# Optimization experiments

Measured on AMD Instinct MI355X. Metric: run time of the kernel, lower is better.

## Reference

```python
import jax, jax.numpy as jnp
import numpy as np

N_GRAPHS = 64
NODES_PER_GRAPH = 1024
N_NODES = N_GRAPHS * NODES_PER_GRAPH
AVG_DEGREE = 32
N_EDGES = N_NODES * AVG_DEGREE
D_FEAT = 256
ALPHA = 0.5
RATIO = 0.5
K = max(int(RATIO * NODES_PER_GRAPH), 1)  # 512 kept nodes per graph


def setup_inputs() -> dict:
    key = jax.random.key(0)
    ks = jax.random.split(key, 6)
    x = jax.random.normal(ks[0], (N_NODES, D_FEAT), dtype=jnp.float32)
    # intra-graph random edges (src, dst local in [0, n), offset by graph id)
    epg = N_EDGES // N_GRAPHS
    src_loc = jax.random.randint(ks[1], (N_EDGES,), 0, NODES_PER_GRAPH, dtype=jnp.int32)
    dst_loc = jax.random.randint(ks[2], (N_EDGES,), 0, NODES_PER_GRAPH, dtype=jnp.int32)
    off = (jnp.arange(N_EDGES, dtype=jnp.int32) // epg) * NODES_PER_GRAPH
    edge_index = jnp.stack([src_loc + off, dst_loc + off])  # [2, E] int32
    batch = jnp.repeat(jnp.arange(N_GRAPHS, dtype=jnp.int32), NODES_PER_GRAPH)
    scale = 1.0 / np.sqrt(D_FEAT)
    w1 = jax.random.normal(ks[3], (D_FEAT, 1), dtype=jnp.float32) * scale
    b1 = jnp.zeros((1,), dtype=jnp.float32)
    wg = jax.random.normal(ks[4], (D_FEAT, 1), dtype=jnp.float32) * scale
    bg = jnp.zeros((1,), dtype=jnp.float32)
    return {"x": x, "edge_index": edge_index, "batch": batch,
            "w1": w1, "b1": b1, "wg": wg, "bg": bg}


def reference(x, edge_index, batch, w1, b1, wg, bg):
    N = x.shape[0]
    row, col = edge_index[0], edge_index[1]
    # remove_self_loops only affects the GCN scoring path
    ew = (row != col).astype(x.dtype)  # zero-weight self loops == removed
    # GCNConv (add_self_loops=False): D^-1/2 A D^-1/2 (X Wg) + bg
    deg = jnp.zeros((N,), x.dtype).at[col].add(ew)
    dis = jnp.where(deg > 0, jax.lax.rsqrt(jnp.maximum(deg, 1.0)), 0.0)
    norm = dis[row] * dis[col] * ew  # [E]
    xw = x @ wg  # [N, 1]
    gcn = jnp.zeros((N, 1), x.dtype).at[col].add(norm[:, None] * xw[row]) + bg
    score = (ALPHA * (x @ w1 + b1) + (1.0 - ALPHA) * gcn).squeeze(-1)  # [N]
    # segmented top-k: equal-sized graphs -> reshape to [B, n]
    sc = score.reshape(N_GRAPHS, NODES_PER_GRAPH)
    _, idx = jax.lax.top_k(sc, K)  # [B, K], descending (matches torch.topk order)
    perm = (idx + (jnp.arange(N_GRAPHS, dtype=idx.dtype) * NODES_PER_GRAPH)[:, None]).reshape(-1)
    x_new = x[perm] * jnp.tanh(score[perm])[:, None]  # [B*K, D]
    batch_new = batch[perm]
    # filter_adj: keep edges with both endpoints selected, relabel by position in perm
    node_map = jnp.full((N,), -1, jnp.int32).at[perm].set(jnp.arange(perm.shape[0], dtype=jnp.int32))
    er, ec = node_map[row], node_map[col]
    valid = (er >= 0) & (ec >= 0)
    new_edge_index = jnp.where(valid[None, :], jnp.stack([er, ec]), -1)  # -1 marks dropped edges
    return x_new, new_edge_index, batch_new
```

## Files before the change

kernel.cpp:

```cpp
#include <hip/hip_runtime.h>

#define NPG 1024
#define NG 64
#define KKEEP 512
#define DF 256
#define NTOT (NG * NPG)
#define NROWS (NG * KKEEP)
#define EPG 32768
#define NBD 4
#define EPBD (EPG / NBD)
#define NB 8
#define EPB (EPG / NB)
#define HI_ROWS 256
#define LO_ROWS (NROWS - HI_ROWS)
#define FXS 1099511627776.0
#define DOTS_BLOCKS (NTOT / 16)

typedef float vf4 __attribute__((ext_vector_type(4)));
typedef int   vi4 __attribute__((ext_vector_type(4)));
typedef unsigned int vu4 __attribute__((ext_vector_type(4)));

__device__ __forceinline__ unsigned long long cex(unsigned long long a, int t, int k, int j) {
    unsigned long long b = __shfl_xor(a, j, 64);
    bool lower = ((t & j) == 0);
    bool desc  = ((t & k) == 0);
    unsigned long long mn = a < b ? a : b;
    unsigned long long mx = a < b ? b : a;
    return (desc == lower) ? mx : mn;
}

__global__ __launch_bounds__(256) void k_front(const float* __restrict__ x,
                                               const float* __restrict__ w1,
                                               const float* __restrict__ wg,
                                               const int* __restrict__ rows,
                                               const int* __restrict__ cols,
                                               float* __restrict__ sc0,
                                               float* __restrict__ xwg,
                                               int* __restrict__ degp,
                                               unsigned int* __restrict__ ep) {
    __shared__ int deg_l[NPG];
    const int b = blockIdx.x;
    const int t = threadIdx.x;
    if (b < DOTS_BLOCKS) {
        const int lane = t & 63;
        const int grp  = lane & 15;
        const int node = b * 16 + (t >> 6) * 4 + (lane >> 4);
        double s1 = 0.0, s2 = 0.0;
#pragma unroll
        for (int i = 0; i < 4; ++i) {
            const int off = grp * 4 + i * 64;
            const float4 xv = *reinterpret_cast<const float4*>(x + (size_t)node * DF + off);
            const float4 av = *reinterpret_cast<const float4*>(w1 + off);
            const float4 bv = *reinterpret_cast<const float4*>(wg + off);
            s1 += (double)xv.x * av.x + (double)xv.y * av.y + (double)xv.z * av.z + (double)xv.w * av.w;
            s2 += (double)xv.x * bv.x + (double)xv.y * bv.y + (double)xv.z * bv.z + (double)xv.w * bv.w;
        }
#pragma unroll
        for (int m = 1; m <= 8; m <<= 1) {
            s1 += __shfl_xor(s1, m);
            s2 += __shfl_xor(s2, m);
        }
        if (grp == 0) { sc0[node] = (float)s1; xwg[node] = (float)s2; }
    } else {
        const int bb = b - DOTS_BLOCKS;
        const int g = bb >> 2, sub = bb & 3;
        deg_l[t] = 0; deg_l[t + 256] = 0; deg_l[t + 512] = 0; deg_l[t + 768] = 0;
        __syncthreads();
        const size_t e0 = (size_t)g * EPG + sub * EPBD;
        const int4* r4 = reinterpret_cast<const int4*>(rows + e0);
        const int4* c4 = reinterpret_cast<const int4*>(cols + e0);
        vu4* ep4 = reinterpret_cast<vu4*>(ep + e0);
#pragma unroll 2
        for (int i = t; i < EPBD / 4; i += 256) {
            int4 r = r4[i], c = c4[i];
            vu4 p;
            p.x = (((unsigned)r.x & (NPG - 1)) << 10) | ((unsigned)c.x & (NPG - 1));
            p.y = (((unsigned)r.y & (NPG - 1)) << 10) | ((unsigned)c.y & (NPG - 1));
            p.z = (((unsigned)r.z & (NPG - 1)) << 10) | ((unsigned)c.z & (NPG - 1));
            p.w = (((unsigned)r.w & (NPG - 1)) << 10) | ((unsigned)c.w & (NPG - 1));
            ep4[i] = p;
            if (r.x != c.x) atomicAdd(&deg_l[p.x & (NPG - 1)], 1);
            if (r.y != c.y) atomicAdd(&deg_l[p.y & (NPG - 1)], 1);
            if (r.z != c.z) atomicAdd(&deg_l[p.z & (NPG - 1)], 1);
            if (r.w != c.w) atomicAdd(&deg_l[p.w & (NPG - 1)], 1);
        }
        __syncthreads();
        int* dst = degp + (size_t)bb * NPG;
        dst[t] = deg_l[t]; dst[t + 256] = deg_l[t + 256];
        dst[t + 512] = deg_l[t + 512]; dst[t + 768] = deg_l[t + 768];
    }
}

__global__ __launch_bounds__(1024) void k_gcn(const unsigned int* __restrict__ ep,
                                              const int* __restrict__ degp,
                                              const float* __restrict__ xwg,
                                              unsigned long long* __restrict__ gcnp) {
    __shared__ float dis_l[NPG];
    __shared__ float dxw_l[NPG];
    __shared__ unsigned long long gcn_l[NPG];
    const int t = threadIdx.x;
    const int g = blockIdx.x >> 3, sub = blockIdx.x & 7;
    {
        int d = degp[(size_t)(g * NBD + 0) * NPG + t] + degp[(size_t)(g * NBD + 1) * NPG + t]
              + degp[(size_t)(g * NBD + 2) * NPG + t] + degp[(size_t)(g * NBD + 3) * NPG + t];
        float dis = (d > 0) ? (1.0f / sqrtf((float)d)) : 0.0f;
        dis_l[t] = dis;
        dxw_l[t] = dis * xwg[g * NPG + t];
    }
    gcn_l[t] = 0;
    __syncthreads();
    const vu4* ep4 = reinterpret_cast<const vu4*>(ep + (size_t)g * EPG + sub * EPB);
    for (int i = t; i < EPB / 4; i += 1024) {
        vu4 p = ep4[i];
        int rl, cl; float term;
        rl = (p.x >> 10) & (NPG - 1); cl = p.x & (NPG - 1);
        if (rl != cl) { term = dxw_l[rl] * dis_l[cl];
            atomicAdd(&gcn_l[cl], (unsigned long long)(long long)llrint((double)term * FXS)); }
        rl = (p.y >> 10) & (NPG - 1); cl = p.y & (NPG - 1);
        if (rl != cl) { term = dxw_l[rl] * dis_l[cl];
            atomicAdd(&gcn_l[cl], (unsigned long long)(long long)llrint((double)term * FXS)); }
        rl = (p.z >> 10) & (NPG - 1); cl = p.z & (NPG - 1);
        if (rl != cl) { term = dxw_l[rl] * dis_l[cl];
            atomicAdd(&gcn_l[cl], (unsigned long long)(long long)llrint((double)term * FXS)); }
        rl = (p.w >> 10) & (NPG - 1); cl = p.w & (NPG - 1);
        if (rl != cl) { term = dxw_l[rl] * dis_l[cl];
            atomicAdd(&gcn_l[cl], (unsigned long long)(long long)llrint((double)term * FXS)); }
    }
    __syncthreads();
    gcnp[(size_t)blockIdx.x * NPG + t] = gcn_l[t];
}

__global__ __launch_bounds__(1024) void k_sort(const float* __restrict__ sc0,
                                               const unsigned long long* __restrict__ gcnp,
                                               const float* __restrict__ b1,
                                               const float* __restrict__ bg,
                                               int* __restrict__ node_map,
                                               int2* __restrict__ rowinfo) {
    __shared__ unsigned long long keys[NPG];
    __shared__ float score_l[NPG];
    const int g = blockIdx.x, t = threadIdx.x;
    const int nbase = g * NPG;
    unsigned long long key;
    {
        long long q = 0;
#pragma unroll
        for (int p = 0; p < NB; ++p) q += (long long)gcnp[(size_t)(g * NB + p) * NPG + t];
        float s2 = (float)((double)q * (1.0 / FXS)) + bg[0];
        float s1 = sc0[nbase + t] + b1[0];
        float s = 0.5f * s1 + 0.5f * s2;
        score_l[t] = s;
        unsigned u = __float_as_uint(s);
        u = (u & 0x80000000u) ? ~u : (u | 0x80000000u);
        key = ((unsigned long long)u << 32) | (unsigned long long)(0xFFFFFFFFu - (unsigned)t);
    }
#pragma unroll
    for (int k = 2; k <= 64; k <<= 1)
        for (int j = k >> 1; j > 0; j >>= 1)
            key = cex(key, t, k, j);
    keys[t] = key;
    __syncthreads();
    for (int k = 128; k <= NPG; k <<= 1) {
        for (int j = k >> 1; j >= 64; j >>= 1) {
            int ixj = t ^ j;
            if (ixj > t) {
                unsigned long long a = keys[t], b = keys[ixj];
                bool desc = ((t & k) == 0);
                if (desc ? (a < b) : (a > b)) { keys[t] = b; keys[ixj] = a; }
            }
            __syncthreads();
        }
        key = keys[t];
#pragma unroll
        for (int j = 32; j > 0; j >>= 1)
            key = cex(key, t, k, j);
        if (k < NPG) { keys[t] = key; __syncthreads(); }
    }
    int idx = (int)(0xFFFFFFFFu - (unsigned)(key & 0xFFFFFFFFull)) & (NPG - 1);
    if (t < KKEEP) {
        int row = g * KKEEP + t;
        node_map[nbase + idx] = row;
        rowinfo[row] = make_int2(nbase + idx, __float_as_int(tanhf(score_l[idx])));
    } else {
        node_map[nbase + idx] = -1;
    }
}

__device__ __forceinline__ void edge_body_packed(const unsigned int* __restrict__ ep,
                                                 const int* __restrict__ node_map,
                                                 float* __restrict__ oute, int E, int i) {
    const int* nm = node_map + (i >> 13) * NPG;
    vu4 p = __builtin_nontemporal_load(reinterpret_cast<const vu4*>(ep) + i);
    int ex = nm[(p.x >> 10) & (NPG - 1)], fx = nm[p.x & (NPG - 1)];
    int ey = nm[(p.y >> 10) & (NPG - 1)], fy = nm[p.y & (NPG - 1)];
    int ez = nm[(p.z >> 10) & (NPG - 1)], fz = nm[p.z & (NPG - 1)];
    int ew = nm[(p.w >> 10) & (NPG - 1)], fw = nm[p.w & (NPG - 1)];
    vf4 orow, ocol;
    orow.x = (ex >= 0 && fx >= 0) ? (float)ex : -1.0f;  ocol.x = (ex >= 0 && fx >= 0) ? (float)fx : -1.0f;
    orow.y = (ey >= 0 && fy >= 0) ? (float)ey : -1.0f;  ocol.y = (ey >= 0 && fy >= 0) ? (float)fy : -1.0f;
    orow.z = (ez >= 0 && fz >= 0) ? (float)ez : -1.0f;  ocol.z = (ez >= 0 && fz >= 0) ? (float)fz : -1.0f;
    orow.w = (ew >= 0 && fw >= 0) ? (float)ew : -1.0f;  ocol.w = (ew >= 0 && fw >= 0) ? (float)fw : -1.0f;
    __builtin_nontemporal_store(orow, reinterpret_cast<vf4*>(oute) + i);
    __builtin_nontemporal_store(ocol, reinterpret_cast<vf4*>(oute + (size_t)E) + i);
}

__device__ __forceinline__ void edge_body_raw(const int* __restrict__ rows,
                                              const int* __restrict__ cols,
                                              const int* __restrict__ node_map,
                                              float* __restrict__ oute, int E, int i) {
    vi4 r = __builtin_nontemporal_load(reinterpret_cast<const vi4*>(rows) + i);
    vi4 c = __builtin_nontemporal_load(reinterpret_cast<const vi4*>(cols) + i);
    int ex = node_map[r.x & (NTOT - 1)], fx = node_map[c.x & (NTOT - 1)];
    int ey = node_map[r.y & (NTOT - 1)], fy = node_map[c.y & (NTOT - 1)];
    int ez = node_map[r.z & (NTOT - 1)], fz = node_map[c.z & (NTOT - 1)];
    int ew = node_map[r.w & (NTOT - 1)], fw = node_map[c.w & (NTOT - 1)];
    vf4 orow, ocol;
    orow.x = (ex >= 0 && fx >= 0) ? (float)ex : -1.0f;  ocol.x = (ex >= 0 && fx >= 0) ? (float)fx : -1.0f;
    orow.y = (ey >= 0 && fy >= 0) ? (float)ey : -1.0f;  ocol.y = (ey >= 0 && fy >= 0) ? (float)fy : -1.0f;
    orow.z = (ez >= 0 && fz >= 0) ? (float)ez : -1.0f;  ocol.z = (ez >= 0 && fz >= 0) ? (float)fz : -1.0f;
    orow.w = (ew >= 0 && fw >= 0) ? (float)ew : -1.0f;  ocol.w = (ew >= 0 && fw >= 0) ? (float)fw : -1.0f;
    __builtin_nontemporal_store(orow, reinterpret_cast<vf4*>(oute) + i);
    __builtin_nontemporal_store(ocol, reinterpret_cast<vf4*>(oute + (size_t)E) + i);
}

__device__ __forceinline__ void gather_row(const float* __restrict__ x, int2 ri, int row,
                                           float* __restrict__ outx, float* __restrict__ outb,
                                           int lane) {
    float tg = __int_as_float(ri.y);
    const float4 v = *reinterpret_cast<const float4*>(x + (size_t)(ri.x & (NTOT - 1)) * DF + lane * 4);
    vf4 o;
    o.x = v.x * tg; o.y = v.y * tg; o.z = v.z * tg; o.w = v.w * tg;
    __builtin_nontemporal_store(o, reinterpret_cast<vf4*>(outx + (size_t)row * DF) + lane);
    if (lane == 0) __builtin_nontemporal_store((float)(row >> 9), outb + row);
}

__global__ __launch_bounds__(256) void k_out(const float* __restrict__ x,
                                             const unsigned int* __restrict__ ep,
                                             const int* __restrict__ rows,
                                             const int* __restrict__ cols,
                                             const int* __restrict__ node_map,
                                             const int2* __restrict__ rowinfo,
                                             float* __restrict__ outx,
                                             float* __restrict__ oute,
                                             float* __restrict__ outb, int E) {
    const int b = blockIdx.x, t = threadIdx.x;
    if (b < NROWS / 4) {
        int row = b * 4 + (t >> 6);
        gather_row(x, rowinfo[row], row, outx, outb, t & 63);
    } else {
        int i = (b - NROWS / 4) * 256 + t;
        if (i < E / 4) {
            if (ep) edge_body_packed(ep, node_map, oute, E, i);
            else    edge_body_raw(rows, cols, node_map, oute, E, i);
        }
    }
}

__global__ __launch_bounds__(256) void k_edges(const unsigned int* __restrict__ ep,
                                               const int* __restrict__ node_map,
                                               float* __restrict__ oute, int E) {
    int i = blockIdx.x * blockDim.x + threadIdx.x;
    if (i < E / 4) edge_body_packed(ep, node_map, oute, E, i);
}

__global__ __launch_bounds__(256) void k_gather(const float* __restrict__ x,
                                                const int2* __restrict__ rowinfo,
                                                float* __restrict__ outx,
                                                float* __restrict__ outb) {
    int row = blockIdx.x * 4 + (threadIdx.x >> 6);
    gather_row(x, rowinfo[row], row, outx, outb, threadIdx.x & 63);
}

__global__ __launch_bounds__(1024) void k_gather_hi(const float* __restrict__ x,
                                                    const int2* __restrict__ rowinfo,
                                                    float* __restrict__ outx,
                                                    float* __restrict__ outb) {
    __shared__ int2 info[HI_ROWS];
    int tid = threadIdx.x;
    if (tid < HI_ROWS) info[tid] = rowinfo[LO_ROWS + tid];
    __syncthreads();
    for (int it = tid; it < HI_ROWS * 64; it += 1024) {
        int rl = it >> 6, lane = it & 63;
        gather_row(x, info[rl], LO_ROWS + rl, outx, outb, lane);
    }
}

extern "C" void kernel_launch(void* const* d_in, const int* in_sizes, int n_in,
                              void* d_out, int out_size, void* d_ws, size_t ws_size,
                              hipStream_t stream) {
    const float* x = (const float*)d_in[0];
    const int* ei = (const int*)d_in[1];
    const float* w1 = (const float*)d_in[3];
    const float* b1 = (const float*)d_in[4];
    const float* wg = (const float*)d_in[5];
    const float* bg = (const float*)d_in[6];

    const int N = in_sizes[0] / DF;
    const int E = in_sizes[1] / 2;
    const int* rows = ei;
    const int* cols = ei + E;

    float* outx = (float*)d_out;
    float* oute = outx + (size_t)NROWS * DF;
    float* outb = oute + (size_t)2 * E;

    char* sb = (char*)d_out;
    float*              sc0  = (float*)(sb + 0);
    float*              xwg  = (float*)(sb + (1 << 18));
    int*                degp = (int*)(sb + (2 << 18));
    unsigned long long* gcnp = (unsigned long long*)(sb + (6 << 18));

    const size_t EPBYTES = (size_t)E * 4;
    int tier;
    int*  node_map;
    int2* rowinfo;
    unsigned int* ep;
    unsigned int* ep_out;
    if (ws_size >= (size_t)NTOT * 4 + (size_t)NROWS * 8 + EPBYTES) {
        tier = 1;
        node_map = (int*)d_ws;
        rowinfo  = (int2*)((char*)d_ws + (size_t)NTOT * 4);
        ep       = (unsigned int*)((char*)d_ws + (size_t)NTOT * 4 + (size_t)NROWS * 8);
        ep_out   = ep;
    } else if (ws_size >= (size_t)NTOT * 4 + (size_t)NROWS * 8) {
        tier = 1;
        node_map = (int*)d_ws;
        rowinfo  = (int2*)((char*)d_ws + (size_t)NTOT * 4);
        ep       = (unsigned int*)(sb + (22 << 18));
        ep_out   = nullptr;
    } else if (ws_size >= (size_t)NROWS * 8) {
        tier = 2;
        node_map = (int*)(sb + (54 << 18));
        rowinfo  = (int2*)d_ws;
        ep       = (unsigned int*)(sb + (22 << 18));
        ep_out   = ep;
    } else {
        tier = 3;
        node_map = (int*)(sb + (54 << 18));
        rowinfo  = (int2*)(sb + (size_t)NROWS * DF * 4 - (size_t)NROWS * 8);
        ep       = (unsigned int*)(sb + (22 << 18));
        ep_out   = ep;
    }

    hipLaunchKernelGGL(k_front, dim3(DOTS_BLOCKS + NG * NBD), dim3(256), 0, stream,
                       x, w1, wg, rows, cols, sc0, xwg, degp, ep);
    hipLaunchKernelGGL(k_gcn, dim3(NG * NB), dim3(1024), 0, stream, ep, degp, xwg, gcnp);
    hipLaunchKernelGGL(k_sort, dim3(NG), dim3(1024), 0, stream, sc0, gcnp, b1, bg, node_map, rowinfo);
    if (tier == 1) {
        hipLaunchKernelGGL(k_out, dim3(NROWS / 4 + E / 4 / 256), dim3(256), 0, stream,
                           x, ep_out, rows, cols, node_map, rowinfo, outx, oute, outb, E);
    } else if (tier == 2) {
        hipLaunchKernelGGL(k_edges, dim3(E / 4 / 256), dim3(256), 0, stream, ep_out, node_map, oute, E);
        hipLaunchKernelGGL(k_gather, dim3(NROWS / 4), dim3(256), 0, stream, x, rowinfo, outx, outb);
    } else {
        hipLaunchKernelGGL(k_edges, dim3(E / 4 / 256), dim3(256), 0, stream, ep_out, node_map, oute, E);
        hipLaunchKernelGGL(k_gather, dim3(LO_ROWS / 4), dim3(256), 0, stream, x, rowinfo, outx, outb);
        hipLaunchKernelGGL(k_gather_hi, dim3(1), dim3(1024), 0, stream, x, rowinfo, outx, outb);
    }
}
```

Measured before the change: 52.67 us.

## Fuse GCN aggregation and per-graph sort into one kernel per graph

Merges the GCN scatter kernel (8 blocks per graph) and the top-k sort kernel into a single kernel with one 1024-thread block per graph. The gcn partial sums stay in shared memory, and that buffer is reused for the sort keys. This removes the gcnp round trip through global memory and one kernel launch. The cost is less parallelism for the edge aggregation: 64 blocks instead of 512, each walking 32K edges. Edge index loads in k_front are also switched to nontemporal loads.

```diff
diff --git a/kernel.cpp b/kernel.cpp
--- a/kernel.cpp
+++ b/kernel.cpp
@@ -9,8 +9,6 @@
 #define EPG 32768
 #define NBD 4
 #define EPBD (EPG / NBD)
-#define NB 8
-#define EPB (EPG / NB)
 #define HI_ROWS 256
 #define LO_ROWS (NROWS - HI_ROWS)
 #define FXS 1099511627776.0
@@ -67,12 +65,13 @@
         deg_l[t] = 0; deg_l[t + 256] = 0; deg_l[t + 512] = 0; deg_l[t + 768] = 0;
         __syncthreads();
         const size_t e0 = (size_t)g * EPG + sub * EPBD;
-        const int4* r4 = reinterpret_cast<const int4*>(rows + e0);
-        const int4* c4 = reinterpret_cast<const int4*>(cols + e0);
+        const vi4* r4 = reinterpret_cast<const vi4*>(rows + e0);
+        const vi4* c4 = reinterpret_cast<const vi4*>(cols + e0);
         vu4* ep4 = reinterpret_cast<vu4*>(ep + e0);
 #pragma unroll 2
         for (int i = t; i < EPBD / 4; i += 256) {
-            int4 r = r4[i], c = c4[i];
+            vi4 r = __builtin_nontemporal_load(r4 + i);
+            vi4 c = __builtin_nontemporal_load(c4 + i);
             vu4 p;
             p.x = (((unsigned)r.x & (NPG - 1)) << 10) | ((unsigned)c.x & (NPG - 1));
             p.y = (((unsigned)r.y & (NPG - 1)) << 10) | ((unsigned)c.y & (NPG - 1));
@@ -91,26 +90,31 @@
     }
 }
 
-__global__ __launch_bounds__(1024) void k_gcn(const unsigned int* __restrict__ ep,
-                                              const int* __restrict__ degp,
-                                              const float* __restrict__ xwg,
-                                              unsigned long long* __restrict__ gcnp) {
+__global__ __launch_bounds__(1024) void k_gs(const unsigned int* __restrict__ ep,
+                                             const int* __restrict__ degp,
+                                             const float* __restrict__ xwg,
+                                             const float* __restrict__ sc0,
+                                             const float* __restrict__ b1,
+                                             const float* __restrict__ bg,
+                                             int* __restrict__ node_map,
+                                             int2* __restrict__ rowinfo) {
     __shared__ float dis_l[NPG];
     __shared__ float dxw_l[NPG];
     __shared__ unsigned long long gcn_l[NPG];
-    const int t = threadIdx.x;
-    const int g = blockIdx.x >> 3, sub = blockIdx.x & 7;
+    __shared__ float score_l[NPG];
+    const int g = blockIdx.x, t = threadIdx.x;
+    const int nbase = g * NPG;
     {
         int d = degp[(size_t)(g * NBD + 0) * NPG + t] + degp[(size_t)(g * NBD + 1) * NPG + t]
               + degp[(size_t)(g * NBD + 2) * NPG + t] + degp[(size_t)(g * NBD + 3) * NPG + t];
         float dis = (d > 0) ? (1.0f / sqrtf((float)d)) : 0.0f;
         dis_l[t] = dis;
-        dxw_l[t] = dis * xwg[g * NPG + t];
+        dxw_l[t] = dis * xwg[nbase + t];
     }
     gcn_l[t] = 0;
     __syncthreads();
-    const vu4* ep4 = reinterpret_cast<const vu4*>(ep + (size_t)g * EPG + sub * EPB);
-    for (int i = t; i < EPB / 4; i += 1024) {
+    const vu4* ep4 = reinterpret_cast<const vu4*>(ep + (size_t)g * EPG);
+    for (int i = t; i < EPG / 4; i += 1024) {
         vu4 p = ep4[i];
         int rl, cl; float term;
         rl = (p.x >> 10) & (NPG - 1); cl = p.x & (NPG - 1);
@@ -127,25 +131,9 @@
             atomicAdd(&gcn_l[cl], (unsigned long long)(long long)llrint((double)term * FXS)); }
     }
     __syncthreads();
-    gcnp[(size_t)blockIdx.x * NPG + t] = gcn_l[t];
-}
-
-__global__ __launch_bounds__(1024) void k_sort(const float* __restrict__ sc0,
-                                               const unsigned long long* __restrict__ gcnp,
-                                               const float* __restrict__ b1,
-                                               const float* __restrict__ bg,
-                                               int* __restrict__ node_map,
-                                               int2* __restrict__ rowinfo) {
-    __shared__ unsigned long long keys[NPG];
-    __shared__ float score_l[NPG];
-    const int g = blockIdx.x, t = threadIdx.x;
-    const int nbase = g * NPG;
     unsigned long long key;
     {
-        long long q = 0;
-#pragma unroll
-        for (int p = 0; p < NB; ++p) q += (long long)gcnp[(size_t)(g * NB + p) * NPG + t];
-        float s2 = (float)((double)q * (1.0 / FXS)) + bg[0];
+        float s2 = (float)((double)(long long)gcn_l[t] * (1.0 / FXS)) + bg[0];
         float s1 = sc0[nbase + t] + b1[0];
         float s = 0.5f * s1 + 0.5f * s2;
         score_l[t] = s;
@@ -157,23 +145,23 @@
     for (int k = 2; k <= 64; k <<= 1)
         for (int j = k >> 1; j > 0; j >>= 1)
             key = cex(key, t, k, j);
-    keys[t] = key;
+    gcn_l[t] = key;
     __syncthreads();
     for (int k = 128; k <= NPG; k <<= 1) {
         for (int j = k >> 1; j >= 64; j >>= 1) {
             int ixj = t ^ j;
             if (ixj > t) {
-                unsigned long long a = keys[t], b = keys[ixj];
+                unsigned long long a = gcn_l[t], b = gcn_l[ixj];
                 bool desc = ((t & k) == 0);
-                if (desc ? (a < b) : (a > b)) { keys[t] = b; keys[ixj] = a; }
+                if (desc ? (a < b) : (a > b)) { gcn_l[t] = b; gcn_l[ixj] = a; }
             }
             __syncthreads();
         }
-        key = keys[t];
+        key = gcn_l[t];
 #pragma unroll
         for (int j = 32; j > 0; j >>= 1)
             key = cex(key, t, k, j);
-        if (k < NPG) { keys[t] = key; __syncthreads(); }
+        if (k < NPG) { gcn_l[t] = key; __syncthreads(); }
     }
     int idx = (int)(0xFFFFFFFFu - (unsigned)(key & 0xFFFFFFFFull)) & (NPG - 1);
     if (t < KKEEP) {
@@ -304,10 +292,9 @@
     float* outb = oute + (size_t)2 * E;
 
     char* sb = (char*)d_out;
-    float*              sc0  = (float*)(sb + 0);
-    float*              xwg  = (float*)(sb + (1 << 18));
-    int*                degp = (int*)(sb + (2 << 18));
-    unsigned long long* gcnp = (unsigned long long*)(sb + (6 << 18));
+    float* sc0  = (float*)(sb + 0);
+    float* xwg  = (float*)(sb + (1 << 18));
+    int*   degp = (int*)(sb + (2 << 18));
 
     const size_t EPBYTES = (size_t)E * 4;
     int tier;
@@ -325,26 +312,26 @@
         tier = 1;
         node_map = (int*)d_ws;
         rowinfo  = (int2*)((char*)d_ws + (size_t)NTOT * 4);
-        ep       = (unsigned int*)(sb + (22 << 18));
+        ep       = (unsigned int*)(sb + (6 << 18));
         ep_out   = nullptr;
     } else if (ws_size >= (size_t)NROWS * 8) {
         tier = 2;
-        node_map = (int*)(sb + (54 << 18));
+        node_map = (int*)(sb + (38 << 18));
         rowinfo  = (int2*)d_ws;
-        ep       = (unsigned int*)(sb + (22 << 18));
+        ep       = (unsigned int*)(sb + (6 << 18));
         ep_out   = ep;
     } else {
         tier = 3;
-        node_map = (int*)(sb + (54 << 18));
+        node_map = (int*)(sb + (38 << 18));
         rowinfo  = (int2*)(sb + (size_t)NROWS * DF * 4 - (size_t)NROWS * 8);
-        ep       = (unsigned int*)(sb + (22 << 18));
+        ep       = (unsigned int*)(sb + (6 << 18));
         ep_out   = ep;
     }
 
     hipLaunchKernelGGL(k_front, dim3(DOTS_BLOCKS + NG * NBD), dim3(256), 0, stream,
                        x, w1, wg, rows, cols, sc0, xwg, degp, ep);
-    hipLaunchKernelGGL(k_gcn, dim3(NG * NB), dim3(1024), 0, stream, ep, degp, xwg, gcnp);
-    hipLaunchKernelGGL(k_sort, dim3(NG), dim3(1024), 0, stream, sc0, gcnp, b1, bg, node_map, rowinfo);
+    hipLaunchKernelGGL(k_gs, dim3(NG), dim3(1024), 0, stream,
+                       ep, degp, xwg, sc0, b1, bg, node_map, rowinfo);
     if (tier == 1) {
         hipLaunchKernelGGL(k_out, dim3(NROWS / 4 + E / 4 / 256), dim3(256), 0, stream,
                            x, ep_out, rows, cols, node_map, rowinfo, outx, oute, outb, E);
```

Measured after the change: 54.52 us. 3.5% more time.
